# Kernel optimization log

Measured on AMD Instinct MI355X. Metric: run time of the kernel, lower is better.

## Reference

```python
import jax, jax.numpy as jnp
import numpy as np

B, N, DIM = 8, 2048, 1024
NUM_HEADS = 16
HEAD_DIM = DIM // NUM_HEADS
LOW_RANK = 5
RANK_MULTI = 2


def setup_inputs() -> dict:
    key = jax.random.key(0)
    ks = jax.random.split(key, 12)
    r, rm, H, D = LOW_RANK, LOW_RANK * RANK_MULTI, NUM_HEADS, HEAD_DIM
    return {
        "x": jax.random.normal(ks[0], (B, N, DIM), jnp.float32),
        "inputs_mask": jnp.ones((B, N), jnp.float32),
        "eps": jax.random.normal(ks[1], (B, H, N, r), jnp.float32),
        "qk_w": jax.random.normal(ks[2], (2 * DIM, DIM), jnp.float32) * 0.02,
        "we_p": jax.random.normal(ks[3], (H, rm, r), jnp.float32) * 0.3,
        "wr_p": jax.random.normal(ks[4], (H, rm, r), jnp.float32) * 0.3,
        "log_lam": jax.random.uniform(ks[5], (H, r), jnp.float32),
        "m_u": jax.random.normal(ks[6], (1, H, r, r), jnp.float32),
        "s_tri": jax.random.normal(ks[7], (1, H, r, r, r), jnp.float32),
        "log_ssqrt": jax.random.normal(ks[8], (1, H, r, r), jnp.float32),
        "fw_w": jax.random.normal(ks[9], (HEAD_DIM, r), jnp.float32) * 0.1,
        "fw_b": jnp.zeros((HEAD_DIM,), jnp.float32),
    }


def _l2norm(v):
    # F.normalize(v, p=2, dim=-1) with eps=1e-12
    return v / jnp.maximum(jnp.linalg.norm(v, axis=-1, keepdims=True), 1e-12)


def reference(x, inputs_mask, eps, qk_w, we_p, wr_p, log_lam, m_u, s_tri, log_ssqrt, fw_w, fw_b):
    Bx, Nx, C = x.shape
    H, rm, r = we_p.shape
    D = C // H
    # qk projection: [B,N,2C] -> q,k [B,H,N,D]
    qk = (x @ qk_w.T).reshape(Bx, Nx, 2, H, D).transpose(2, 0, 3, 1, 4)
    q, k = qk[0], qk[1]
    mask = inputs_mask[:, None, :, None]  # [B,1,N,1]
    # gen_weights: rm evenly spaced tokens -> data-dependent low-rank maps
    idx = jnp.linspace(0, Nx - 1, rm).astype(jnp.int32)
    xs = x.reshape(Bx, Nx, H, D).transpose(0, 2, 3, 1)[:, :, :, idx]  # [B,H,D,rm]
    we = jnp.einsum('bhdm,hmr->bhdr', xs, we_p)
    wr = jnp.einsum('bhdm,hmr->bhdr', xs, wr_p)
    q = _l2norm(q * mask)
    k = _l2norm(k * mask)
    escore = jnp.einsum('bhnd,bhdr->bhnr', q, we)  # [B,H,N,r]
    rscore = jnp.einsum('bhnd,bhdr->bhnr', k, wr)
    lam2 = jnp.exp(2.0 * log_lam)  # diag(exp(log_lam))**2, [H,r]
    v1 = (escore + rscore) * lam2[None, :, None, :]  # [B,H,N,r]
    mean = jnp.einsum('bhna,has->bhns', v1, m_u[0])
    # S[h,a,b,c] = diag_embed(exp(log_ssqrt)) + tril(s_tri, -1)
    r_eye = jnp.eye(r, dtype=x.dtype)
    tril_mask = jnp.tril(jnp.ones((r, r), x.dtype), -1)
    S = jnp.exp(log_ssqrt[0])[..., None] * r_eye + s_tri[0] * tril_mask  # [H,r,r,r]
    # noise[b,h,n,c] = sum_{a,u} v1[b,h,n,a] S[h,a,u,c] eps[b,h,n,u]
    noise = jnp.einsum('bhna,hauc,bhnu->bhnc', v1, S, eps)
    samples = mean + noise  # [B,H,N,r]
    attn_out = jnp.einsum('bhnr,dr->bhnd', samples, fw_w) + fw_b
    attn_out = attn_out.transpose(0, 2, 1, 3).reshape(Bx, Nx, C)
    # KL divergence
    kl = 0.5 * jnp.sum((lam2[:, :, None, None] * S) ** 2)
    kl += 0.5 * jnp.sum(jnp.exp(4.0 * log_lam)[:, :, None] * m_u[0] ** 2)
    kl -= jnp.sum(log_ssqrt)
    kl -= 2.0 * jnp.sum(log_lam) * r
    kl -= 0.5 * r * r * H
    return attn_out, escore, rscore, kl
```

## Files before the change

### kernel.cpp

```cpp
#include <hip/hip_runtime.h>
#include <math.h>

#define Bv 8
#define Nv 2048
#define DIMv 1024
#define Hv 16
#define Dv 64
#define Rv 5
#define RMv 10

#define ATTN_OFF 0
#define ESC_OFF (Bv * Nv * DIMv)
#define RSC_OFF (ESC_OFF + Bv * Hv * Nv * Rv)
#define KL_OFF  (RSC_OFF + Bv * Hv * Nv * Rv)

#define BMt 128
#define BK 64
#define BUF_BYTES 32768

#define XHALFS (Bv * Nv * DIMv)
#define QKHALFS (2 * DIMv * DIMv)
#define CONV_BLOCKS ((XHALFS + QKHALFS) / 8 / 256)

using half8 = __attribute__((ext_vector_type(8))) _Float16;
using f32x4 = __attribute__((ext_vector_type(4))) float;

#define GLOAD(gp, lp)                                                      \
    __builtin_amdgcn_global_load_lds(                                      \
        (const __attribute__((address_space(1))) void*)(gp),               \
        (__attribute__((address_space(3))) void*)(lp), 16, 0, 0)

__global__ __launch_bounds__(256)
void convert_fp16(const float* __restrict__ x, const float* __restrict__ qk,
                  _Float16* __restrict__ xh, _Float16* __restrict__ qkh,
                  const float* __restrict__ log_lam, const float* __restrict__ m_u,
                  const float* __restrict__ s_tri, const float* __restrict__ log_ssqrt,
                  float* __restrict__ out)
{
    __shared__ float red[256];
    const int t = threadIdx.x;

    if (blockIdx.x == CONV_BLOCKS) {
        float acc = 0.f;
        for (int idx = t; idx < Hv * Rv * Rv * Rv; idx += 256) {
            int hh = idx / 125;
            int rem = idx % 125;
            int a = rem / 25, u = (rem / 5) % 5, c = rem % 5;
            float S = 0.f;
            if (u == c)      S = expf(log_ssqrt[(hh * Rv + a) * Rv + u]);
            else if (u > c)  S = s_tri[((hh * Rv + a) * Rv + u) * Rv + c];
            float lam2 = expf(2.f * log_lam[hh * Rv + a]);
            float z = lam2 * S;
            acc += 0.5f * z * z;
        }
        for (int idx = t; idx < Hv * Rv * Rv; idx += 256) {
            int hh = idx / 25, a = (idx / 5) % 5;
            float e4 = expf(4.f * log_lam[hh * Rv + a]);
            float mu = m_u[idx];
            acc += 0.5f * e4 * mu * mu;
            acc -= log_ssqrt[idx];
        }
        for (int idx = t; idx < Hv * Rv; idx += 256) acc -= 2.f * (float)Rv * log_lam[idx];

        red[t] = acc;
        __syncthreads();
        for (int s = 128; s > 0; s >>= 1) {
            if (t < s) red[t] += red[t + s];
            __syncthreads();
        }
        if (t == 0) out[KL_OFF] = red[0] - 0.5f * (float)(Rv * Rv * Hv);
        return;
    }

    size_t i = ((size_t)blockIdx.x * 256 + t) * 8;
    const float* src;
    _Float16* dst;
    if (i < XHALFS) { src = x + i; dst = xh + i; }
    else            { src = qk + (i - XHALFS); dst = qkh + (i - XHALFS); }
    float4 v0 = *(const float4*)src;
    float4 v1 = *(const float4*)(src + 4);
    half8 hv = {(_Float16)v0.x, (_Float16)v0.y, (_Float16)v0.z, (_Float16)v0.w,
                (_Float16)v1.x, (_Float16)v1.y, (_Float16)v1.z, (_Float16)v1.w};
    *(half8*)dst = hv;
}

__global__ __launch_bounds__(256, 2)
void svgp_main(const _Float16* __restrict__ xh, const _Float16* __restrict__ qkh,
               const float* __restrict__ x, const float* __restrict__ mask,
               const float* __restrict__ eps,
               const float* __restrict__ we_p, const float* __restrict__ wr_p,
               const float* __restrict__ log_lam, const float* __restrict__ m_u,
               const float* __restrict__ s_tri, const float* __restrict__ log_ssqrt,
               const float* __restrict__ fw_w, const float* __restrict__ fw_b,
               float* __restrict__ out)
{
    const int id = blockIdx.x;
    const int h = 2 * (id & 7) + ((id >> 3) & 1);
    const int rowTile = id >> 4;
    const int row0 = rowTile * BMt;
    const int b0 = row0 >> 11;
    const int t = threadIdx.x;
    const int lane = t & 63;
    const int w = t >> 6;
    const int wu = __builtin_amdgcn_readfirstlane(w);
    const int dm = lane & 15;
    const int rg = lane >> 4;

    __shared__ float4 sStageV[4096];
    char* sBytes = (char*)sStageV;
    float (*sRed)[12] = (float (*)[12])sStageV;

    __shared__ float sS[Rv][Rv][Rv];
    __shared__ float sMu[Rv][Rv];
    __shared__ float sFw[Dv][Rv];
    __shared__ float sFb[Dv];
    __shared__ float sLam2[Rv];
    __shared__ float sWe[Dv][Rv];
    __shared__ float sWr[Dv][Rv];

    if (t < 125) {
        int a = t / 25, u = (t % 25) / 5, c = t % 5;
        float v = 0.f;
        if (u == c)      v = expf(log_ssqrt[(h * Rv + a) * Rv + u]);
        else if (u > c)  v = s_tri[((h * Rv + a) * Rv + u) * Rv + c];
        sS[a][u][c] = v;
    }
    if (t >= 128 && t < 153) { int i = t - 128; sMu[i / 5][i % 5] = m_u[h * Rv * Rv + i]; }
    if (t >= 160 && t < 165) sLam2[t - 160] = expf(2.f * log_lam[h * Rv + (t - 160)]);
    if (t >= 192 && t < 256) sFb[t - 192] = fw_b[t - 192];
    if (t < 320) sFw[t / Rv][t % Rv] = fw_w[t];
    { int t2 = t + 256; if (t2 < 320) sFw[t2 / Rv][t2 % Rv] = fw_w[t2]; }

    if (t < 64) {
        float xv[RMv];
#pragma unroll
        for (int m = 0; m < RMv; ++m) {
            int nidx = (m == RMv - 1) ? (Nv - 1) : (int)((float)m * (2047.0f / 9.0f));
            xv[m] = x[((size_t)b0 * Nv + nidx) * DIMv + h * Dv + t];
        }
#pragma unroll
        for (int rr = 0; rr < Rv; ++rr) {
            float sw = 0.f, sr = 0.f;
#pragma unroll
            for (int m = 0; m < RMv; ++m) {
                sw = fmaf(xv[m], we_p[(h * RMv + m) * Rv + rr], sw);
                sr = fmaf(xv[m], wr_p[(h * RMv + m) * Rv + rr], sr);
            }
            sWe[t][rr] = sw; sWr[t][rr] = sr;
        }
    }

    size_t aOff[4], bOff[4];
    int ldsA[4], ldsB[4];
#pragma unroll
    for (int j = 0; j < 4; ++j) {
        int c = wu * 4 + j;
        int s = c * 64 + lane;
        int rl = ((s >> 7) << 4) + (s & 15);
        int ko = (s >> 4) & 7;
        aOff[j] = (size_t)(row0 + rl) * DIMv + ko * 8;
        int grow = (rl < 64) ? (h * Dv + rl) : (DIMv + h * Dv + (rl - 64));
        bOff[j] = (size_t)grow * DIMv + ko * 8;
        ldsA[j] = c * 1024;
        ldsB[j] = 16384 + c * 1024;
    }

    const int wm = wu >> 1, wn = wu & 1;
    f32x4 acc[4][4];
#pragma unroll
    for (int i = 0; i < 4; ++i)
#pragma unroll
        for (int j = 0; j < 4; ++j) acc[i][j] = (f32x4){0.f, 0.f, 0.f, 0.f};

    auto stage = [&](int bb, int kk0) {
#pragma unroll
        for (int j = 0; j < 4; ++j) {
            GLOAD(xh + aOff[j] + kk0, sBytes + bb + ldsA[j]);
            GLOAD(qkh + bOff[j] + kk0, sBytes + bb + ldsB[j]);
        }
    };
    auto compute = [&](int bb) {
        _Float16* sH = (_Float16*)(sBytes + bb);
#pragma unroll
        for (int kk = 0; kk < 2; ++kk) {
            const int fo = (kk * 4 + rg) * 16 + dm;
            half8 af[4], bf[4];
#pragma unroll
            for (int i = 0; i < 4; ++i)
                af[i] = *(half8*)(sH + ((wm * 4 + i) * 128 + fo) * 8);
#pragma unroll
            for (int j = 0; j < 4; ++j)
                bf[j] = *(half8*)(sH + (1024 + (wn * 4 + j) * 128 + fo) * 8);
#pragma unroll
            for (int i = 0; i < 4; ++i)
#pragma unroll
                for (int j = 0; j < 4; ++j)
                    acc[i][j] = __builtin_amdgcn_mfma_f32_16x16x32_f16(af[i], bf[j], acc[i][j], 0, 0, 0);
        }
    };

    stage(0, 0);
    __syncthreads();
    for (int k0 = 0; k0 < DIMv; k0 += 2 * BK) {
        stage(BUF_BYTES, k0 + BK);
        compute(0);
        __syncthreads();
        if (k0 + 2 * BK < DIMv)
            stage(0, k0 + 2 * BK);
        compute(BUF_BYTES);
        __syncthreads();
    }

    {
        const float* sW = wn ? &sWr[0][0] : &sWe[0][0];
        float wv[4][Rv];
#pragma unroll
        for (int j = 0; j < 4; ++j)
#pragma unroll
            for (int r = 0; r < Rv; ++r)
                wv[j][r] = sW[(j * 16 + dm) * Rv + r];

#pragma unroll
        for (int i = 0; i < 4; ++i)
#pragma unroll
            for (int reg = 0; reg < 4; ++reg) {
                float red[6] = {0.f, 0.f, 0.f, 0.f, 0.f, 0.f};
#pragma unroll
                for (int j = 0; j < 4; ++j) {
                    float v = acc[i][j][reg];
                    red[0] = fmaf(v, v, red[0]);
#pragma unroll
                    for (int r = 0; r < Rv; ++r)
                        red[1 + r] = fmaf(v, wv[j][r], red[1 + r]);
                }
#pragma unroll
                for (int off = 8; off > 0; off >>= 1)
#pragma unroll
                    for (int u = 0; u < 6; ++u)
                        red[u] += __shfl_xor(red[u], off, 64);
                if (dm == 0) {
                    const int rowI = wm * 64 + i * 16 + rg * 4 + reg;
#pragma unroll
                    for (int u = 0; u < 6; ++u)
                        sRed[rowI][wn * 6 + u] = red[u];
                }
            }
    }
    __syncthreads();

    const int d0 = dm * 4;
    float fwv[4][Rv], fbv[4];
#pragma unroll
    for (int i = 0; i < 4; ++i) {
        fbv[i] = sFb[d0 + i];
#pragma unroll
        for (int r = 0; r < Rv; ++r) fwv[i][r] = sFw[d0 + i][r];
    }

    for (int p = 0; p < 8; ++p) {
        const int row = w * 32 + p * 4 + rg;
        const int nf = row0 + row;
        const int n = nf & (Nv - 1);
        const float mk = mask[nf];
        const float amk = fabsf(mk);

        const float qn = fmaxf(amk * sqrtf(sRed[row][0]), 1e-12f);
        const float kn = fmaxf(amk * sqrtf(sRed[row][6]), 1e-12f);
        const float iq = mk / qn;
        const float ik = mk / kn;

        float esc[Rv], rsc[Rv], v1[Rv];
#pragma unroll
        for (int r = 0; r < Rv; ++r) {
            esc[r] = sRed[row][1 + r] * iq;
            rsc[r] = sRed[row][7 + r] * ik;
            v1[r] = (esc[r] + rsc[r]) * sLam2[r];
        }

        const size_t eb = (((size_t)(nf >> 11) * Hv + h) * Nv + n) * Rv;
        float ev[Rv];
#pragma unroll
        for (int u = 0; u < Rv; ++u) ev[u] = eps[eb + u];

        float smp[Rv];
#pragma unroll
        for (int c = 0; c < Rv; ++c) {
            float mn = 0.f;
#pragma unroll
            for (int a = 0; a < Rv; ++a) mn = fmaf(v1[a], sMu[a][c], mn);
            float nz = 0.f;
#pragma unroll
            for (int u = 0; u < Rv; ++u) {
                float s = 0.f;
#pragma unroll
                for (int a = 0; a < Rv; ++a) s = fmaf(v1[a], sS[a][u][c], s);
                nz = fmaf(s, ev[u], nz);
            }
            smp[c] = mn + nz;
        }

        float4 ao;
        float aov[4];
#pragma unroll
        for (int i = 0; i < 4; ++i) {
            float a = fbv[i];
#pragma unroll
            for (int r = 0; r < Rv; ++r) a = fmaf(smp[r], fwv[i][r], a);
            aov[i] = a;
        }
        ao.x = aov[0]; ao.y = aov[1]; ao.z = aov[2]; ao.w = aov[3];
        *(float4*)&out[ATTN_OFF + (size_t)nf * DIMv + h * Dv + d0] = ao;

        if (dm == 0) {
#pragma unroll
            for (int r = 0; r < Rv; ++r) {
                out[ESC_OFF + eb + r] = esc[r];
                out[RSC_OFF + eb + r] = rsc[r];
            }
        }
    }
}

extern "C" void kernel_launch(void* const* d_in, const int* in_sizes, int n_in,
                              void* d_out, int out_size, void* d_ws, size_t ws_size,
                              hipStream_t stream) {
    const float* x        = (const float*)d_in[0];
    const float* mask     = (const float*)d_in[1];
    const float* eps      = (const float*)d_in[2];
    const float* qk_w     = (const float*)d_in[3];
    const float* we_p     = (const float*)d_in[4];
    const float* wr_p     = (const float*)d_in[5];
    const float* log_lam  = (const float*)d_in[6];
    const float* m_u      = (const float*)d_in[7];
    const float* s_tri    = (const float*)d_in[8];
    const float* log_ssqrt= (const float*)d_in[9];
    const float* fw_w     = (const float*)d_in[10];
    const float* fw_b     = (const float*)d_in[11];
    float* out = (float*)d_out;

    _Float16* xh  = (_Float16*)d_ws;
    _Float16* qkh = xh + XHALFS;

    convert_fp16<<<dim3(CONV_BLOCKS + 1), 256, 0, stream>>>(x, qk_w, xh, qkh,
                                                            log_lam, m_u, s_tri, log_ssqrt, out);
    svgp_main<<<dim3(2048), 256, 0, stream>>>(xh, qkh, x, mask, eps, we_p, wr_p,
                                              log_lam, m_u, s_tri, log_ssqrt, fw_w, fw_b, out);
}
```

Measured before the change: 359.1 us.

## Halve row tile and use triple-buffered LDS pipeline with explicit vmcnt waits

Shrinks the GEMM row tile from 128 to 64 rows, which doubles the grid to 4096 blocks. It also replaces the double-buffered loop with a three-stage ring that keeps two loads in flight, using explicit s_waitcnt vmcnt counts, raw barriers and sched_barriers. The aim is more parallelism and better overlap of global-to-LDS loads with MFMA work. In exchange, each block re-reads the qk weight tile over half as many rows, roughly doubling B-operand traffic, and the hand-written wait counts must match the number of loads in flight exactly.

After: 409.3 us. +14.0%, slower.

```diff
diff --git a/kernel.cpp b/kernel.cpp
--- a/kernel.cpp
+++ b/kernel.cpp
@@ -14,9 +14,9 @@
 #define RSC_OFF (ESC_OFF + Bv * Hv * Nv * Rv)
 #define KL_OFF  (RSC_OFF + Bv * Hv * Nv * Rv)
 
-#define BMt 128
+#define BMt 64
 #define BK 64
-#define BUF_BYTES 32768
+#define BUF_BYTES 24576
 
 #define XHALFS (Bv * Nv * DIMv)
 #define QKHALFS (2 * DIMv * DIMv)
@@ -29,6 +29,13 @@
     __builtin_amdgcn_global_load_lds(                                      \
         (const __attribute__((address_space(1))) void*)(gp),               \
         (__attribute__((address_space(3))) void*)(lp), 16, 0, 0)
+
+#define VMW12 asm volatile("s_waitcnt vmcnt(12)" ::: "memory")
+#define VMW6  asm volatile("s_waitcnt vmcnt(6)" ::: "memory")
+#define VMW0  asm volatile("s_waitcnt vmcnt(0)" ::: "memory")
+#define LGKM0 asm volatile("s_waitcnt lgkmcnt(0)" ::: "memory")
+#define BAR   __builtin_amdgcn_s_barrier()
+#define SB0   __builtin_amdgcn_sched_barrier(0)
 
 __global__ __launch_bounds__(256)
 void convert_fp16(const float* __restrict__ x, const float* __restrict__ qk,
@@ -96,8 +103,8 @@
 {
     const int id = blockIdx.x;
     const int h = 2 * (id & 7) + ((id >> 3) & 1);
-    const int rowTile = id >> 4;
-    const int row0 = rowTile * BMt;
+    const int rt = id >> 4;
+    const int row0 = rt * BMt;
     const int b0 = row0 >> 11;
     const int t = threadIdx.x;
     const int lane = t & 63;
@@ -106,7 +113,7 @@
     const int dm = lane & 15;
     const int rg = lane >> 4;
 
-    __shared__ float4 sStageV[4096];
+    __shared__ float4 sStageV[4608];
     char* sBytes = (char*)sStageV;
     float (*sRed)[12] = (float (*)[12])sStageV;
 
@@ -150,66 +157,79 @@
         }
     }
 
-    size_t aOff[4], bOff[4];
-    int ldsA[4], ldsB[4];
+    size_t aOff[2], bOff[4];
+    int ldsA[2], ldsB[4];
+#pragma unroll
+    for (int j = 0; j < 2; ++j) {
+        int c = wu * 2 + j;
+        int s = c * 64 + lane;
+        int rl = ((s >> 7) << 4) + (s & 15);
+        int ko = (s >> 4) & 7;
+        aOff[j] = (size_t)(row0 + rl) * DIMv + ko * 8;
+        ldsA[j] = c * 1024;
+    }
 #pragma unroll
     for (int j = 0; j < 4; ++j) {
         int c = wu * 4 + j;
         int s = c * 64 + lane;
         int rl = ((s >> 7) << 4) + (s & 15);
         int ko = (s >> 4) & 7;
-        aOff[j] = (size_t)(row0 + rl) * DIMv + ko * 8;
         int grow = (rl < 64) ? (h * Dv + rl) : (DIMv + h * Dv + (rl - 64));
         bOff[j] = (size_t)grow * DIMv + ko * 8;
-        ldsA[j] = c * 1024;
-        ldsB[j] = 16384 + c * 1024;
+        ldsB[j] = 8192 + c * 1024;
     }
 
     const int wm = wu >> 1, wn = wu & 1;
-    f32x4 acc[4][4];
-#pragma unroll
-    for (int i = 0; i < 4; ++i)
+    f32x4 acc[2][4];
+#pragma unroll
+    for (int i = 0; i < 2; ++i)
 #pragma unroll
         for (int j = 0; j < 4; ++j) acc[i][j] = (f32x4){0.f, 0.f, 0.f, 0.f};
 
     auto stage = [&](int bb, int kk0) {
 #pragma unroll
-        for (int j = 0; j < 4; ++j) {
-            GLOAD(xh + aOff[j] + kk0, sBytes + bb + ldsA[j]);
-            GLOAD(qkh + bOff[j] + kk0, sBytes + bb + ldsB[j]);
-        }
+        for (int j = 0; j < 2; ++j) GLOAD(xh + aOff[j] + kk0, sBytes + bb + ldsA[j]);
+#pragma unroll
+        for (int j = 0; j < 4; ++j) GLOAD(qkh + bOff[j] + kk0, sBytes + bb + ldsB[j]);
     };
     auto compute = [&](int bb) {
         _Float16* sH = (_Float16*)(sBytes + bb);
 #pragma unroll
         for (int kk = 0; kk < 2; ++kk) {
             const int fo = (kk * 4 + rg) * 16 + dm;
-            half8 af[4], bf[4];
-#pragma unroll
-            for (int i = 0; i < 4; ++i)
-                af[i] = *(half8*)(sH + ((wm * 4 + i) * 128 + fo) * 8);
+            half8 af[2], bf[4];
+#pragma unroll
+            for (int i = 0; i < 2; ++i)
+                af[i] = *(half8*)(sH + ((wm * 2 + i) * 128 + fo) * 8);
 #pragma unroll
             for (int j = 0; j < 4; ++j)
-                bf[j] = *(half8*)(sH + (1024 + (wn * 4 + j) * 128 + fo) * 8);
-#pragma unroll
-            for (int i = 0; i < 4; ++i)
+                bf[j] = *(half8*)(sH + (512 + (wn * 4 + j) * 128 + fo) * 8);
+#pragma unroll
+            for (int i = 0; i < 2; ++i)
 #pragma unroll
                 for (int j = 0; j < 4; ++j)
                     acc[i][j] = __builtin_amdgcn_mfma_f32_16x16x32_f16(af[i], bf[j], acc[i][j], 0, 0, 0);
         }
     };
 
+#define PH(bufb, stgb, kidx, WAIT) \
+        stage(stgb, (kidx) * BK); WAIT; BAR; SB0; compute(bufb); LGKM0; SB0; BAR
+#define PHN(bufb, WAIT) \
+        WAIT; BAR; SB0; compute(bufb); LGKM0; SB0; BAR
+
     stage(0, 0);
-    __syncthreads();
-    for (int k0 = 0; k0 < DIMv; k0 += 2 * BK) {
-        stage(BUF_BYTES, k0 + BK);
-        compute(0);
-        __syncthreads();
-        if (k0 + 2 * BK < DIMv)
-            stage(0, k0 + 2 * BK);
-        compute(BUF_BYTES);
-        __syncthreads();
-    }
+    stage(BUF_BYTES, BK);
+    for (int p3 = 0; p3 < 12; p3 += 3) {
+        PH(0,             2 * BUF_BYTES, p3 + 2, VMW12);
+        PH(BUF_BYTES,     0,             p3 + 3, VMW12);
+        PH(2 * BUF_BYTES, BUF_BYTES,     p3 + 4, VMW12);
+    }
+    PH(0,         2 * BUF_BYTES, 14, VMW12);
+    PH(BUF_BYTES, 0,             15, VMW12);
+    PHN(2 * BUF_BYTES, VMW6);
+    PHN(0,             VMW0);
+#undef PH
+#undef PHN
 
     {
         const float* sW = wn ? &sWr[0][0] : &sWe[0][0];
@@ -221,7 +241,7 @@
                 wv[j][r] = sW[(j * 16 + dm) * Rv + r];
 
 #pragma unroll
-        for (int i = 0; i < 4; ++i)
+        for (int i = 0; i < 2; ++i)
 #pragma unroll
             for (int reg = 0; reg < 4; ++reg) {
                 float red[6] = {0.f, 0.f, 0.f, 0.f, 0.f, 0.f};
@@ -239,7 +259,7 @@
                     for (int u = 0; u < 6; ++u)
                         red[u] += __shfl_xor(red[u], off, 64);
                 if (dm == 0) {
-                    const int rowI = wm * 64 + i * 16 + rg * 4 + reg;
+                    const int rowI = wm * 32 + i * 16 + rg * 4 + reg;
 #pragma unroll
                     for (int u = 0; u < 6; ++u)
                         sRed[rowI][wn * 6 + u] = red[u];
@@ -257,8 +277,8 @@
         for (int r = 0; r < Rv; ++r) fwv[i][r] = sFw[d0 + i][r];
     }
 
-    for (int p = 0; p < 8; ++p) {
-        const int row = w * 32 + p * 4 + rg;
+    for (int p = 0; p < 4; ++p) {
+        const int row = w * 16 + p * 4 + rg;
         const int nf = row0 + row;
         const int n = nf & (Nv - 1);
         const float mk = mask[nf];
@@ -343,6 +363,6 @@
 
     convert_fp16<<<dim3(CONV_BLOCKS + 1), 256, 0, stream>>>(x, qk_w, xh, qkh,
                                                             log_lam, m_u, s_tri, log_ssqrt, out);
-    svgp_main<<<dim3(2048), 256, 0, stream>>>(xh, qkh, x, mask, eps, we_p, wr_p,
+    svgp_main<<<dim3(4096), 256, 0, stream>>>(xh, qkh, x, mask, eps, we_p, wr_p,
                                               log_lam, m_u, s_tri, log_ssqrt, fw_w, fw_b, out);
 }
```
